# Optimization experiments

Hardware: AMD Instinct MI355X
Metric: run time of the kernel (lower is better)

## Reference

```python
import jax, jax.numpy as jnp
import numpy as np

N_NODES = 50000
N_EDGES = 800000


def _sage_mean(x, src, dst, w, W_self, W_neigh, b, n_nodes):
    # DGL SAGEConv('mean') with edge_weight: messages m_e = w_e * h[src_e],
    # h_neigh[v] = sum_{e->v} m_e / in_degree(v)  (zero if no in-edges),
    # out = h @ W_self + h_neigh @ W_neigh + b
    msg = x[src] * w[:, None]                                   # [E, d]
    s = jax.ops.segment_sum(msg, dst, num_segments=n_nodes)     # [N, d]
    deg = jax.ops.segment_sum(jnp.ones_like(w), dst, num_segments=n_nodes)
    h_neigh = s / jnp.clip(deg, 1.0)[:, None]
    return x @ W_self + h_neigh @ W_neigh + b


def setup_inputs() -> dict:
    key = jax.random.key(0)
    ks = jax.random.split(key, 12)
    d_in, d_h = 64, 256
    inp = {
        'features': jax.random.normal(ks[0], (N_NODES, d_in), dtype=jnp.float32),
        'edge_src': jax.random.randint(ks[1], (N_EDGES,), 0, N_NODES, dtype=jnp.int32),
        'edge_dst': jax.random.randint(ks[2], (N_EDGES,), 0, N_NODES, dtype=jnp.int32),
        'edge_weights': jax.random.uniform(ks[3], (N_EDGES,), dtype=jnp.float32),
        'W1_self': jax.random.normal(ks[4], (d_in, d_h), dtype=jnp.float32) * (1.0 / np.sqrt(d_in)),
        'W1_neigh': jax.random.normal(ks[5], (d_in, d_h), dtype=jnp.float32) * (1.0 / np.sqrt(d_in)),
        'b1': jnp.zeros((d_h,), dtype=jnp.float32),
        'W2_self': jax.random.normal(ks[6], (d_h, 128), dtype=jnp.float32) * (1.0 / np.sqrt(d_h)),
        'W2_neigh': jax.random.normal(ks[7], (d_h, 128), dtype=jnp.float32) * (1.0 / np.sqrt(d_h)),
        'b2': jnp.zeros((128,), dtype=jnp.float32),
        'Wl1': jax.random.normal(ks[8], (128, 64), dtype=jnp.float32) * (1.0 / np.sqrt(128)),
        'bl1': jnp.zeros((64,), dtype=jnp.float32),
        'Wl2': jax.random.normal(ks[9], (64, 32), dtype=jnp.float32) * (1.0 / np.sqrt(64)),
        'bl2': jnp.zeros((32,), dtype=jnp.float32),
        'Wl3': jax.random.normal(ks[10], (32, 10), dtype=jnp.float32) * (1.0 / np.sqrt(32)),
        'bl3': jnp.zeros((10,), dtype=jnp.float32),
    }
    return inp


def reference(features, edge_src, edge_dst, edge_weights,
              W1_self, W1_neigh, b1, W2_self, W2_neigh, b2,
              Wl1, bl1, Wl2, bl2, Wl3, bl3):
    n = features.shape[0]
    x = features.reshape(n, -1)  # flatten (already 2D)
    x = jax.nn.relu(_sage_mean(x, edge_src, edge_dst, edge_weights,
                               W1_self, W1_neigh, b1, n))
    # conv2 is applied twice on identical inputs in the original; results are equal
    embeddings = _sage_mean(x, edge_src, edge_dst, edge_weights,
                            W2_self, W2_neigh, b2, n)
    h = jax.nn.relu(embeddings @ Wl1 + bl1)
    h = jax.nn.relu(h @ Wl2 + bl2)
    out = h @ Wl3 + bl3
    return (out, embeddings)
```

## Files before the change

kernel.cpp:

```cpp
#include <hip/hip_runtime.h>
#include <hip/hip_bf16.h>

#define N_NODES 50000
#define N_EDGES 800000
#define MT_TILES 3125
#define PR_TILES 1563

#define NBLK_SORT 200
#define CHUNK_SORT 4000
#define NBKT 196

typedef __attribute__((ext_vector_type(8))) short frag_ab;
typedef __attribute__((ext_vector_type(4))) float frag_cd;

static __device__ __forceinline__ unsigned short f2b(float f) {
    union { float f; unsigned u; } v; v.f = f;
    unsigned r = v.u + 0x7fffu + ((v.u >> 16) & 1u);
    return (unsigned short)(r >> 16);
}
static __device__ __forceinline__ float b2f(unsigned short b) {
    union { float f; unsigned u; } v; v.u = ((unsigned)b) << 16;
    return v.f;
}
static __device__ __forceinline__ float blo(unsigned p) { return b2f((unsigned short)(p & 0xffffu)); }
static __device__ __forceinline__ float bhi(unsigned p) { return b2f((unsigned short)(p >> 16)); }

static __device__ __forceinline__ unsigned short packBK_elem(const float* __restrict__ Wa,
                                                             const float* __restrict__ Wb,
                                                             int Ka, int N, int idx) {
    int j = idx & 7;
    int lane = (idx >> 3) & 63;
    int rest = idx >> 9;
    int ntiles = N >> 4;
    int nt = rest % ntiles;
    int kt = rest / ntiles;
    int kk = kt * 32 + (lane >> 4) * 8 + j;
    int nn = nt * 16 + (lane & 15);
    float v = (kk < Ka) ? Wa[kk * N + nn] : Wb[(kk - Ka) * N + nn];
    return f2b(v);
}
static __device__ __forceinline__ unsigned short packBN_elem(const float* __restrict__ Wa,
                                                             const float* __restrict__ Wb,
                                                             int Na, int N, int idx) {
    int j = idx & 7;
    int lane = (idx >> 3) & 63;
    int rest = idx >> 9;
    int ntiles = N >> 4;
    int nt = rest % ntiles;
    int kt = rest / ntiles;
    int kk = kt * 32 + (lane >> 4) * 8 + j;
    int nn = nt * 16 + (lane & 15);
    float v = (nn < Na) ? Wa[kk * Na + nn] : Wb[kk * (N - Na) + (nn - Na)];
    return f2b(v);
}

#define PREP_S0 800000
#define PREP_S1 (PREP_S0 + 32768)
#define PREP_S2 (PREP_S1 + 65536)
#define PREP_S3 (PREP_S2 + 8192)
#define PREP_S4 (PREP_S3 + 2048)
#define PREP_BLKS 3549

__global__ __launch_bounds__(256) void prep_p1_kernel(const float4* __restrict__ x4,
                                                      ushort4* __restrict__ xb4,
                                                      const float* __restrict__ W1s,
                                                      const float* __restrict__ W1n,
                                                      const float* __restrict__ W2s,
                                                      const float* __restrict__ W2n,
                                                      const float* __restrict__ Wl1,
                                                      const float* __restrict__ Wl2,
                                                      unsigned short* __restrict__ B1p,
                                                      unsigned short* __restrict__ B2p,
                                                      unsigned short* __restrict__ Bl1p,
                                                      unsigned short* __restrict__ Bl2p,
                                                      const int* __restrict__ dst,
                                                      int* __restrict__ G) {
    __shared__ int h[256];
    int bid = blockIdx.x;
    int t = threadIdx.x;
    if (bid >= PREP_BLKS) {
        int blk = bid - PREP_BLKS;
        h[t] = 0;
        __syncthreads();
        int base = blk * CHUNK_SORT;
        for (int i = t; i < CHUNK_SORT; i += 256)
            atomicAdd(&h[dst[base + i] >> 8], 1);
        __syncthreads();
        G[blk * 256 + t] = h[t];
        return;
    }
    int idx = bid * 256 + t;
    if (idx < PREP_S0) {
        float4 v = x4[idx];
        ushort4 o;
        o.x = f2b(v.x); o.y = f2b(v.y); o.z = f2b(v.z); o.w = f2b(v.w);
        xb4[idx] = o;
    } else if (idx < PREP_S1) {
        int i = idx - PREP_S0;
        B1p[i] = packBK_elem(W1s, W1n, 64, 256, i);
    } else if (idx < PREP_S2) {
        int i = idx - PREP_S1;
        B2p[i] = packBN_elem(W2s, W2n, 128, 256, i);
    } else if (idx < PREP_S3) {
        int i = idx - PREP_S2;
        Bl1p[i] = packBK_elem(Wl1, Wl1, 128, 64, i);
    } else {
        int i = idx - PREP_S3;
        Bl2p[i] = packBK_elem(Wl2, Wl2, 64, 32, i);
    }
}


__global__ __launch_bounds__(256) void p2a_scan(int* __restrict__ G,
                                                int* __restrict__ colsum) {
    __shared__ int sc[256];
    int b = blockIdx.x;
    int t = threadIdx.x;
    int v = (t < NBLK_SORT) ? G[t * 256 + b] : 0;
    sc[t] = v;
    __syncthreads();
    for (int off = 1; off < 256; off <<= 1) {
        int add = (t >= off) ? sc[t - off] : 0;
        __syncthreads();
        sc[t] += add;
        __syncthreads();
    }
    if (t < NBLK_SORT) G[t * 256 + b] = sc[t] - v;
    if (t == 255) colsum[b] = sc[255];
}

__global__ __launch_bounds__(256) void p2b_scan(const int* __restrict__ colsum,
                                                int* __restrict__ bucket_off,
                                                int* __restrict__ row_off) {
    __shared__ int sc[256];
    int t = threadIdx.x;
    int v = colsum[t];
    sc[t] = v;
    __syncthreads();
    for (int off = 1; off < 256; off <<= 1) {
        int add = (t >= off) ? sc[t - off] : 0;
        __syncthreads();
        sc[t] += add;
        __syncthreads();
    }
    bucket_off[t] = sc[t] - v;
    if (t == 255) row_off[N_NODES] = sc[255];
}

__global__ __launch_bounds__(256) void p3_scatter(const int* __restrict__ src,
                                                  const int* __restrict__ dst,
                                                  const float* __restrict__ w,
                                                  const int* __restrict__ G,
                                                  const int* __restrict__ bucket_off,
                                                  int* __restrict__ bdst,
                                                  int2* __restrict__ bsedge) {
    __shared__ int cur[256];
    int t = threadIdx.x;
    cur[t] = G[blockIdx.x * 256 + t] + bucket_off[t];
    __syncthreads();
    int base = blockIdx.x * CHUNK_SORT;
    for (int i = t; i < CHUNK_SORT; i += 256) {
        int e = base + i;
        int d = dst[e];
        int pos = atomicAdd(&cur[d >> 8], 1);
        bdst[pos] = d;
        bsedge[pos] = make_int2(src[e], __float_as_int(w[e]));
    }
}

__global__ __launch_bounds__(256) void p4_sort(const int* __restrict__ bucket_off,
                                               const int* __restrict__ bdst,
                                               const int2* __restrict__ bsedge,
                                               int* __restrict__ row_off,
                                               float* __restrict__ inv_deg,
                                               int2* __restrict__ sedge) {
    __shared__ int lcnt[256];
    __shared__ int lcur[256];
    __shared__ int sc[256];
    int t = threadIdx.x;
    int b = blockIdx.x;
    int e0 = bucket_off[b], e1 = bucket_off[b + 1];
    int d0 = b << 8;
    lcnt[t] = 0;
    __syncthreads();
    for (int e = e0 + t; e < e1; e += 256)
        atomicAdd(&lcnt[bdst[e] - d0], 1);
    __syncthreads();
    int v = lcnt[t];
    sc[t] = v;
    __syncthreads();
    for (int off = 1; off < 256; off <<= 1) {
        int add = (t >= off) ? sc[t - off] : 0;
        __syncthreads();
        sc[t] += add;
        __syncthreads();
    }
    int loff = e0 + sc[t] - v;
    lcur[t] = loff;
    int d = d0 + t;
    if (d < N_NODES) {
        row_off[d] = loff;
        inv_deg[d] = 1.0f / (float)(v > 0 ? v : 1);
    }
    __syncthreads();
    for (int e = e0 + t; e < e1; e += 256) {
        int dd = bdst[e];
        int2 sv = bsedge[e];
        int pos = atomicAdd(&lcur[dd - d0], 1);
        sedge[pos] = sv;
    }
}


__global__ __launch_bounds__(256) void agg64_kernel(const uint4* __restrict__ xb4,
                                                    const int* __restrict__ row_off,
                                                    const int2* __restrict__ sedge,
                                                    const float* __restrict__ inv_deg,
                                                    uint4* __restrict__ hn1b4) {
    int tid = threadIdx.x;
    int lane = tid & 63;
    int er = lane >> 3;
    int l7 = lane & 7;
    int n = blockIdx.x * 4 + (tid >> 6);
    if (n >= N_NODES) return;
    int e0 = row_off[n], e1 = row_off[n + 1];
    float id = inv_deg[n];
    float a[8];
    #pragma unroll
    for (int j = 0; j < 8; j++) a[j] = 0.f;
    int e1m1 = e1 - 1;
    for (int e = e0; e < e1; e += 16) {
        int2 m[2];
        uint4 p[2];
        float w[2];
        #pragma unroll
        for (int k = 0; k < 2; k++) {
            int ee = e + k * 8 + er;
            int idx = ee < e1 ? ee : e1m1;
            m[k] = sedge[idx];
        }
        #pragma unroll
        for (int k = 0; k < 2; k++) {
            p[k] = xb4[m[k].x * 8 + l7];
            int ee = e + k * 8 + er;
            w[k] = (ee < e1) ? __int_as_float(m[k].y) : 0.f;
        }
        #pragma unroll
        for (int k = 0; k < 2; k++) {
            a[0] += w[k] * blo(p[k].x); a[1] += w[k] * bhi(p[k].x);
            a[2] += w[k] * blo(p[k].y); a[3] += w[k] * bhi(p[k].y);
            a[4] += w[k] * blo(p[k].z); a[5] += w[k] * bhi(p[k].z);
            a[6] += w[k] * blo(p[k].w); a[7] += w[k] * bhi(p[k].w);
        }
    }
    #pragma unroll
    for (int j = 0; j < 8; j++) {
        a[j] += __shfl_xor(a[j], 8, 64);
        a[j] += __shfl_xor(a[j], 16, 64);
        a[j] += __shfl_xor(a[j], 32, 64);
    }
    if (er == 0) {
        uint4 o;
        o.x = (unsigned)f2b(a[0] * id) | ((unsigned)f2b(a[1] * id) << 16);
        o.y = (unsigned)f2b(a[2] * id) | ((unsigned)f2b(a[3] * id) << 16);
        o.z = (unsigned)f2b(a[4] * id) | ((unsigned)f2b(a[5] * id) << 16);
        o.w = (unsigned)f2b(a[6] * id) | ((unsigned)f2b(a[7] * id) << 16);
        hn1b4[n * 8 + l7] = o;
    }
}

__global__ __launch_bounds__(256) void agg128_kernel(const uint4* __restrict__ zb4,
                                                     const int* __restrict__ row_off,
                                                     const int2* __restrict__ sedge,
                                                     const float* __restrict__ inv_deg,
                                                     float* __restrict__ emb,
                                                     uint4* __restrict__ embb4) {
    int tid = threadIdx.x;
    int lane = tid & 63;
    int qr = lane >> 4;
    int l15 = lane & 15;
    int n = blockIdx.x * 4 + (tid >> 6);
    if (n >= N_NODES) return;
    int e0 = row_off[n], e1 = row_off[n + 1];
    float id = inv_deg[n];
    float4 s0, s1;
    if (qr == 0) {
        s0 = ((const float4*)emb)[n * 32 + l15 * 2];
        s1 = ((const float4*)emb)[n * 32 + l15 * 2 + 1];
    }
    float a[8];
    #pragma unroll
    for (int j = 0; j < 8; j++) a[j] = 0.f;
    int e1m1 = e1 - 1;
    for (int e = e0; e < e1; e += 16) {
        int2 m[4];
        uint4 p[4];
        float w[4];
        #pragma unroll
        for (int k = 0; k < 4; k++) {
            int ee = e + k * 4 + qr;
            int idx = ee < e1 ? ee : e1m1;
            m[k] = sedge[idx];
        }
        #pragma unroll
        for (int k = 0; k < 4; k++) {
            p[k] = zb4[m[k].x * 16 + l15];
            int ee = e + k * 4 + qr;
            w[k] = (ee < e1) ? __int_as_float(m[k].y) : 0.f;
        }
        #pragma unroll
        for (int k = 0; k < 4; k++) {
            a[0] += w[k] * blo(p[k].x); a[1] += w[k] * bhi(p[k].x);
            a[2] += w[k] * blo(p[k].y); a[3] += w[k] * bhi(p[k].y);
            a[4] += w[k] * blo(p[k].z); a[5] += w[k] * bhi(p[k].z);
            a[6] += w[k] * blo(p[k].w); a[7] += w[k] * bhi(p[k].w);
        }
    }
    #pragma unroll
    for (int j = 0; j < 8; j++) {
        a[j] += __shfl_xor(a[j], 16, 64);
        a[j] += __shfl_xor(a[j], 32, 64);
    }
    if (qr == 0) {
        float v0 = s0.x + a[0] * id;
        float v1 = s0.y + a[1] * id;
        float v2 = s0.z + a[2] * id;
        float v3 = s0.w + a[3] * id;
        float v4 = s1.x + a[4] * id;
        float v5 = s1.y + a[5] * id;
        float v6 = s1.z + a[6] * id;
        float v7 = s1.w + a[7] * id;
        ((float4*)emb)[n * 32 + l15 * 2]     = make_float4(v0, v1, v2, v3);
        ((float4*)emb)[n * 32 + l15 * 2 + 1] = make_float4(v4, v5, v6, v7);
        uint4 o;
        o.x = (unsigned)f2b(v0) | ((unsigned)f2b(v1) << 16);
        o.y = (unsigned)f2b(v2) | ((unsigned)f2b(v3) << 16);
        o.z = (unsigned)f2b(v4) | ((unsigned)f2b(v5) << 16);
        o.w = (unsigned)f2b(v6) | ((unsigned)f2b(v7) << 16);
        embb4[n * 16 + l15] = o;
    }
}


__global__ __launch_bounds__(256) void gemm1_mfma(const unsigned short* __restrict__ xb,
                                                  const unsigned short* __restrict__ hn1b,
                                                  const unsigned short* __restrict__ Bp,
                                                  const float* __restrict__ b1,
                                                  unsigned short* __restrict__ x1b) {
    __shared__ __align__(16) unsigned short sB[8192];
    int tid = threadIdx.x;
    int lane = tid & 63;
    int wv = tid >> 6;
    int mt = blockIdx.x * 4 + wv;
    if (mt >= MT_TILES) mt = MT_TILES - 1;
    int q = lane >> 4;
    int rl = lane & 15;
    int row = mt * 16 + rl;
    frag_ab a[4];
    a[0] = *(const frag_ab*)(xb + row * 64 + q * 8);
    a[1] = *(const frag_ab*)(xb + row * 64 + q * 8 + 32);
    a[2] = *(const frag_ab*)(hn1b + row * 64 + q * 8);
    a[3] = *(const frag_ab*)(hn1b + row * 64 + q * 8 + 32);
    frag_cd acc[16];
    #pragma unroll
    for (int nt = 0; nt < 16; nt++) acc[nt] = (frag_cd){0.f, 0.f, 0.f, 0.f};
    #pragma unroll
    for (int kt = 0; kt < 4; kt++) {
        __syncthreads();
        #pragma unroll
        for (int i = 0; i < 4; i++) {
            int idx = i * 256 + tid;
            ((float4*)sB)[idx] = ((const float4*)(Bp + kt * 8192))[idx];
        }
        __syncthreads();
        #pragma unroll
        for (int nt = 0; nt < 16; nt++) {
            frag_ab b = *(const frag_ab*)(sB + (nt * 64 + lane) * 8);
            acc[nt] = __builtin_amdgcn_mfma_f32_16x16x32_bf16(a[kt], b, acc[nt], 0, 0, 0);
        }
    }
    int r0 = mt * 16;
    #pragma unroll
    for (int nt = 0; nt < 16; nt++) {
        int c = nt * 16 + rl;
        float bias = b1[c];
        #pragma unroll
        for (int i = 0; i < 4; i++) {
            int r = r0 + q * 4 + i;
            float v = acc[nt][i] + bias;
            v = v > 0.f ? v : 0.f;
            x1b[r * 256 + c] = f2b(v);
        }
    }
}

__global__ __launch_bounds__(256) void gemm2_mfma(const unsigned short* __restrict__ x1b,
                                                  const unsigned short* __restrict__ Bp,
                                                  const float* __restrict__ b2,
                                                  float* __restrict__ emb,
                                                  unsigned short* __restrict__ zb) {
    __shared__ __align__(16) unsigned short sB[8192];
    int tid = threadIdx.x;
    int lane = tid & 63;
    int wv = tid >> 6;
    int mt = blockIdx.x * 4 + wv;
    if (mt >= MT_TILES) mt = MT_TILES - 1;
    int q = lane >> 4;
    int rl = lane & 15;
    int row = mt * 16 + rl;
    const unsigned short* arow = x1b + row * 256 + q * 8;
    frag_ab a[8];
    #pragma unroll
    for (int kt = 0; kt < 8; kt++) a[kt] = *(const frag_ab*)(arow + kt * 32);
    frag_cd acc[16];
    #pragma unroll
    for (int nt = 0; nt < 16; nt++) acc[nt] = (frag_cd){0.f, 0.f, 0.f, 0.f};
    #pragma unroll
    for (int kt = 0; kt < 8; kt++) {
        __syncthreads();
        #pragma unroll
        for (int i = 0; i < 4; i++) {
            int idx = i * 256 + tid;
            ((float4*)sB)[idx] = ((const float4*)(Bp + kt * 8192))[idx];
        }
        __syncthreads();
        #pragma unroll
        for (int nt = 0; nt < 16; nt++) {
            frag_ab b = *(const frag_ab*)(sB + (nt * 64 + lane) * 8);
            acc[nt] = __builtin_amdgcn_mfma_f32_16x16x32_bf16(a[kt], b, acc[nt], 0, 0, 0);
        }
    }
    int r0 = mt * 16;
    #pragma unroll
    for (int nt = 0; nt < 8; nt++) {
        int c = nt * 16 + rl;
        float bias = b2[c];
        #pragma unroll
        for (int i = 0; i < 4; i++) {
            int r = r0 + q * 4 + i;
            emb[r * 128 + c] = acc[nt][i] + bias;
        }
    }
    #pragma unroll
    for (int nt = 8; nt < 16; nt++) {
        int c = (nt - 8) * 16 + rl;
        #pragma unroll
        for (int i = 0; i < 4; i++) {
            int r = r0 + q * 4 + i;
            zb[r * 128 + c] = f2b(acc[nt][i]);
        }
    }
}

__global__ __launch_bounds__(256) void mlp1_mfma(const unsigned short* __restrict__ embb,
                                                 const unsigned short* __restrict__ Bp,
                                                 const float* __restrict__ bl1,
                                                 unsigned short* __restrict__ h64b) {
    int tid = threadIdx.x;
    int lane = tid & 63;
    int wv = tid >> 6;
    int pr = blockIdx.x * 4 + wv;
    if (pr >= PR_TILES) pr = PR_TILES - 1;
    int mt0 = pr * 2;
    int mt1 = mt0 + 1; if (mt1 >= MT_TILES) mt1 = MT_TILES - 1;
    int q = lane >> 4;
    int rl = lane & 15;
    const unsigned short* a0row = embb + (mt0 * 16 + rl) * 128 + q * 8;
    const unsigned short* a1row = embb + (mt1 * 16 + rl) * 128 + q * 8;
    const frag_ab* bp = (const frag_ab*)Bp;
    frag_cd acc0[4], acc1[4];
    #pragma unroll
    for (int nt = 0; nt < 4; nt++) {
        acc0[nt] = (frag_cd){0.f, 0.f, 0.f, 0.f};
        acc1[nt] = (frag_cd){0.f, 0.f, 0.f, 0.f};
    }
    #pragma unroll
    for (int kt = 0; kt < 4; kt++) {
        frag_ab a0 = *(const frag_ab*)(a0row + kt * 32);
        frag_ab a1 = *(const frag_ab*)(a1row + kt * 32);
        #pragma unroll
        for (int nt = 0; nt < 4; nt++) {
            frag_ab b = bp[(kt * 4 + nt) * 64 + lane];
            acc0[nt] = __builtin_amdgcn_mfma_f32_16x16x32_bf16(a0, b, acc0[nt], 0, 0, 0);
            acc1[nt] = __builtin_amdgcn_mfma_f32_16x16x32_bf16(a1, b, acc1[nt], 0, 0, 0);
        }
    }
    int r0a = mt0 * 16 + q * 4, r0b = mt1 * 16 + q * 4;
    #pragma unroll
    for (int nt = 0; nt < 4; nt++) {
        int c = nt * 16 + rl;
        float bias = bl1[c];
        #pragma unroll
        for (int i = 0; i < 4; i++) {
            float v0 = acc0[nt][i] + bias;
            float v1 = acc1[nt][i] + bias;
            h64b[(r0a + i) * 64 + c] = f2b(v0 > 0.f ? v0 : 0.f);
            h64b[(r0b + i) * 64 + c] = f2b(v1 > 0.f ? v1 : 0.f);
        }
    }
}

__global__ __launch_bounds__(256) void mlp23_mfma(const unsigned short* __restrict__ h64b,
                                                  const unsigned short* __restrict__ Bp,
                                                  const float* __restrict__ bl2,
                                                  const float* __restrict__ Wl3,
                                                  const float* __restrict__ bl3,
                                                  float* __restrict__ out) {
    __shared__ float hs[64][33];
    int tid = threadIdx.x;
    int lane = tid & 63;
    int wv = tid >> 6;
    int mt = blockIdx.x * 4 + wv;
    if (mt >= MT_TILES) mt = MT_TILES - 1;
    int q = lane >> 4;
    int rl = lane & 15;
    const unsigned short* arow = h64b + (mt * 16 + rl) * 64 + q * 8;
    const frag_ab* bp = (const frag_ab*)Bp;
    frag_cd acc[2];
    #pragma unroll
    for (int nt = 0; nt < 2; nt++) acc[nt] = (frag_cd){0.f, 0.f, 0.f, 0.f};
    #pragma unroll
    for (int kt = 0; kt < 2; kt++) {
        frag_ab a = *(const frag_ab*)(arow + kt * 32);
        #pragma unroll
        for (int nt = 0; nt < 2; nt++) {
            frag_ab b = bp[(kt * 2 + nt) * 64 + lane];
            acc[nt] = __builtin_amdgcn_mfma_f32_16x16x32_bf16(a, b, acc[nt], 0, 0, 0);
        }
    }
    #pragma unroll
    for (int nt = 0; nt < 2; nt++) {
        int c = nt * 16 + rl;
        float bias = bl2[c];
        #pragma unroll
        for (int i = 0; i < 4; i++) {
            int lr = wv * 16 + q * 4 + i;
            float v = acc[nt][i] + bias;
            hs[lr][c] = v > 0.f ? v : 0.f;
        }
    }
    __syncthreads();
    int base = blockIdx.x * 64;
    for (int idx = tid; idx < 640; idx += 256) {
        int lr = idx / 10;
        int j = idx - lr * 10;
        int n = base + lr;
        if (n < N_NODES) {
            float a = bl3[j];
            #pragma unroll
            for (int k = 0; k < 32; k++) a += hs[lr][k] * Wl3[k * 10 + j];
            out[n * 10 + j] = a;
        }
    }
}


extern "C" void kernel_launch(void* const* d_in, const int* in_sizes, int n_in,
                              void* d_out, int out_size, void* d_ws, size_t ws_size,
                              hipStream_t stream) {
    const float* x   = (const float*)d_in[0];
    const int* esrc  = (const int*)d_in[1];
    const int* edst  = (const int*)d_in[2];
    const float* ew  = (const float*)d_in[3];
    const float* W1s = (const float*)d_in[4];
    const float* W1n = (const float*)d_in[5];
    const float* b1  = (const float*)d_in[6];
    const float* W2s = (const float*)d_in[7];
    const float* W2n = (const float*)d_in[8];
    const float* b2  = (const float*)d_in[9];
    const float* Wl1 = (const float*)d_in[10];
    const float* bl1 = (const float*)d_in[11];
    const float* Wl2 = (const float*)d_in[12];
    const float* bl2 = (const float*)d_in[13];
    const float* Wl3 = (const float*)d_in[14];
    const float* bl3 = (const float*)d_in[15];

    float* out = (float*)d_out;
    float* emb = out + 500000;

    char* ws = (char*)d_ws;
    size_t off = 0;
    auto alloc = [&](size_t bytes) -> void* {
        void* p = ws + off;
        off = (off + bytes + 255) & ~(size_t)255;
        return p;
    };
    int*   row_off = (int*)alloc((size_t)(N_NODES + 1) * 4);
    float* inv_deg = (float*)alloc((size_t)N_NODES * 4);
    int*   G       = (int*)alloc((size_t)NBLK_SORT * 256 * 4);
    int*   colsum  = (int*)alloc(256 * 4);
    int*   bkt_off = (int*)alloc(257 * 4);
    int*   bdst    = (int*)alloc((size_t)N_EDGES * 4);
    int2*  bsedge  = (int2*)alloc((size_t)N_EDGES * 8);
    int2*  sedge   = (int2*)alloc((size_t)N_EDGES * 8);
    unsigned short* xb   = (unsigned short*)alloc((size_t)N_NODES * 64 * 2);
    unsigned short* hn1b = (unsigned short*)alloc((size_t)N_NODES * 64 * 2);
    unsigned short* x1b  = (unsigned short*)alloc((size_t)N_NODES * 256 * 2);
    unsigned short* zb   = (unsigned short*)alloc((size_t)N_NODES * 128 * 2);
    unsigned short* embb = (unsigned short*)alloc((size_t)N_NODES * 128 * 2);
    unsigned short* h64b = (unsigned short*)alloc((size_t)N_NODES * 64 * 2);
    unsigned short* B1p  = (unsigned short*)alloc(128 * 256 * 2);
    unsigned short* B2p  = (unsigned short*)alloc(256 * 256 * 2);
    unsigned short* Bl1p = (unsigned short*)alloc(128 * 64 * 2);
    unsigned short* Bl2p = (unsigned short*)alloc(64 * 32 * 2);

    prep_p1_kernel<<<PREP_BLKS + NBLK_SORT, 256, 0, stream>>>(
        (const float4*)x, (ushort4*)xb, W1s, W1n, W2s, W2n, Wl1, Wl2,
        B1p, B2p, Bl1p, Bl2p, edst, G);

    p2a_scan<<<256, 256, 0, stream>>>(G, colsum);
    p2b_scan<<<1, 256, 0, stream>>>(colsum, bkt_off, row_off);
    p3_scatter<<<NBLK_SORT, 256, 0, stream>>>(esrc, edst, ew, G, bkt_off, bdst, bsedge);
    p4_sort<<<NBKT, 256, 0, stream>>>(bkt_off, bdst, bsedge, row_off, inv_deg, sedge);

    const int PBLK = (PR_TILES + 3) / 4;
    const int GBLK = (MT_TILES + 3) / 4;
    const int ABLK = (N_NODES + 3) / 4;

    agg64_kernel<<<ABLK, 256, 0, stream>>>((const uint4*)xb, row_off, sedge,
                                           inv_deg, (uint4*)hn1b);
    gemm1_mfma<<<GBLK, 256, 0, stream>>>(xb, hn1b, B1p, b1, x1b);

    gemm2_mfma<<<GBLK, 256, 0, stream>>>(x1b, B2p, b2, emb, zb);
    agg128_kernel<<<ABLK, 256, 0, stream>>>((const uint4*)zb, row_off, sedge,
                                            inv_deg, emb, (uint4*)embb);

    mlp1_mfma<<<PBLK, 256, 0, stream>>>(embb, Bl1p, bl1, h64b);
    mlp23_mfma<<<GBLK, 256, 0, stream>>>(h64b, Bl2p, bl2, Wl3, bl3, out);
}
```

Measured before the change: 269.3 us.

## Fold bucket scan into scatter/sort, double-buffer GEMM weights, fuse MLP layers

The single-block bucket-offset scan is removed; p3_scatter and p4_sort now each recompute the 256-entry prefix sum of colsum in shared memory, saving one launch. gemm1 and gemm2 move to 512-thread blocks with double-buffered shared-memory weight tiles, prefetching the next K-slice into registers while the MFMAs run, so each K step needs one barrier instead of two. The three MLP layers run in one kernel that keeps the 64-wide hidden activations in shared memory, dropping the h64b round trip through global memory and one launch. In exchange the scan work is repeated in every scatter and sort block, and the GEMM blocks use more LDS and more threads per block.

```diff
diff --git a/kernel.cpp b/kernel.cpp
--- a/kernel.cpp
+++ b/kernel.cpp
@@ -4,7 +4,6 @@
 #define N_NODES 50000
 #define N_EDGES 800000
 #define MT_TILES 3125
-#define PR_TILES 1563
 
 #define NBLK_SORT 200
 #define CHUNK_SORT 4000
@@ -129,9 +128,14 @@
     if (t == 255) colsum[b] = sc[255];
 }
 
-__global__ __launch_bounds__(256) void p2b_scan(const int* __restrict__ colsum,
-                                                int* __restrict__ bucket_off,
-                                                int* __restrict__ row_off) {
+__global__ __launch_bounds__(256) void p3_scatter(const int* __restrict__ src,
+                                                  const int* __restrict__ dst,
+                                                  const float* __restrict__ w,
+                                                  const int* __restrict__ G,
+                                                  const int* __restrict__ colsum,
+                                                  int* __restrict__ bdst,
+                                                  int2* __restrict__ bsedge) {
+    __shared__ int cur[256];
     __shared__ int sc[256];
     int t = threadIdx.x;
     int v = colsum[t];
@@ -143,20 +147,7 @@
         sc[t] += add;
         __syncthreads();
     }
-    bucket_off[t] = sc[t] - v;
-    if (t == 255) row_off[N_NODES] = sc[255];
-}
-
-__global__ __launch_bounds__(256) void p3_scatter(const int* __restrict__ src,
-                                                  const int* __restrict__ dst,
-                                                  const float* __restrict__ w,
-                                                  const int* __restrict__ G,
-                                                  const int* __restrict__ bucket_off,
-                                                  int* __restrict__ bdst,
-                                                  int2* __restrict__ bsedge) {
-    __shared__ int cur[256];
-    int t = threadIdx.x;
-    cur[t] = G[blockIdx.x * 256 + t] + bucket_off[t];
+    cur[t] = G[blockIdx.x * 256 + t] + (sc[t] - v);
     __syncthreads();
     int base = blockIdx.x * CHUNK_SORT;
     for (int i = t; i < CHUNK_SORT; i += 256) {
@@ -168,7 +159,7 @@
     }
 }
 
-__global__ __launch_bounds__(256) void p4_sort(const int* __restrict__ bucket_off,
+__global__ __launch_bounds__(256) void p4_sort(const int* __restrict__ colsum,
                                                const int* __restrict__ bdst,
                                                const int2* __restrict__ bsedge,
                                                int* __restrict__ row_off,
@@ -177,12 +168,23 @@
     __shared__ int lcnt[256];
     __shared__ int lcur[256];
     __shared__ int sc[256];
+    __shared__ int sE0, sE1;
     int t = threadIdx.x;
     int b = blockIdx.x;
-    int e0 = bucket_off[b], e1 = bucket_off[b + 1];
+    int cv = colsum[t];
+    sc[t] = cv;
+    __syncthreads();
+    for (int off = 1; off < 256; off <<= 1) {
+        int add = (t >= off) ? sc[t - off] : 0;
+        __syncthreads();
+        sc[t] += add;
+        __syncthreads();
+    }
+    if (t == b) { sE0 = sc[t] - cv; sE1 = sc[t]; }
+    lcnt[t] = 0;
+    __syncthreads();
+    int e0 = sE0, e1 = sE1;
     int d0 = b << 8;
-    lcnt[t] = 0;
-    __syncthreads();
     for (int e = e0 + t; e < e1; e += 256)
         atomicAdd(&lcnt[bdst[e] - d0], 1);
     __syncthreads();
@@ -202,6 +204,7 @@
         row_off[d] = loff;
         inv_deg[d] = 1.0f / (float)(v > 0 ? v : 1);
     }
+    if (b == 0 && t == 0) row_off[N_NODES] = N_EDGES;
     __syncthreads();
     for (int e = e0 + t; e < e1; e += 256) {
         int dd = bdst[e];
@@ -342,16 +345,16 @@
 }
 
 
-__global__ __launch_bounds__(256) void gemm1_mfma(const unsigned short* __restrict__ xb,
+__global__ __launch_bounds__(512) void gemm1_mfma(const unsigned short* __restrict__ xb,
                                                   const unsigned short* __restrict__ hn1b,
                                                   const unsigned short* __restrict__ Bp,
                                                   const float* __restrict__ b1,
                                                   unsigned short* __restrict__ x1b) {
-    __shared__ __align__(16) unsigned short sB[8192];
+    __shared__ __align__(16) unsigned short sB[2][8192];
     int tid = threadIdx.x;
     int lane = tid & 63;
     int wv = tid >> 6;
-    int mt = blockIdx.x * 4 + wv;
+    int mt = blockIdx.x * 8 + wv;
     if (mt >= MT_TILES) mt = MT_TILES - 1;
     int q = lane >> 4;
     int rl = lane & 15;
@@ -364,19 +367,23 @@
     frag_cd acc[16];
     #pragma unroll
     for (int nt = 0; nt < 16; nt++) acc[nt] = (frag_cd){0.f, 0.f, 0.f, 0.f};
+    const float4* gB = (const float4*)Bp;
+    float4 s0 = gB[tid], s1 = gB[512 + tid];
+    ((float4*)sB[0])[tid] = s0;
+    ((float4*)sB[0])[512 + tid] = s1;
     #pragma unroll
     for (int kt = 0; kt < 4; kt++) {
         __syncthreads();
-        #pragma unroll
-        for (int i = 0; i < 4; i++) {
-            int idx = i * 256 + tid;
-            ((float4*)sB)[idx] = ((const float4*)(Bp + kt * 8192))[idx];
-        }
-        __syncthreads();
+        if (kt < 3) { s0 = gB[(kt + 1) * 1024 + tid]; s1 = gB[(kt + 1) * 1024 + 512 + tid]; }
+        const unsigned short* sb = sB[kt & 1];
         #pragma unroll
         for (int nt = 0; nt < 16; nt++) {
-            frag_ab b = *(const frag_ab*)(sB + (nt * 64 + lane) * 8);
+            frag_ab b = *(const frag_ab*)(sb + (nt * 64 + lane) * 8);
             acc[nt] = __builtin_amdgcn_mfma_f32_16x16x32_bf16(a[kt], b, acc[nt], 0, 0, 0);
+        }
+        if (kt < 3) {
+            ((float4*)sB[(kt + 1) & 1])[tid] = s0;
+            ((float4*)sB[(kt + 1) & 1])[512 + tid] = s1;
         }
     }
     int r0 = mt * 16;
@@ -394,16 +401,16 @@
     }
 }
 
-__global__ __launch_bounds__(256) void gemm2_mfma(const unsigned short* __restrict__ x1b,
+__global__ __launch_bounds__(512) void gemm2_mfma(const unsigned short* __restrict__ x1b,
                                                   const unsigned short* __restrict__ Bp,
                                                   const float* __restrict__ b2,
                                                   float* __restrict__ emb,
                                                   unsigned short* __restrict__ zb) {
-    __shared__ __align__(16) unsigned short sB[8192];
+    __shared__ __align__(16) unsigned short sB[2][8192];
     int tid = threadIdx.x;
     int lane = tid & 63;
     int wv = tid >> 6;
-    int mt = blockIdx.x * 4 + wv;
+    int mt = blockIdx.x * 8 + wv;
     if (mt >= MT_TILES) mt = MT_TILES - 1;
     int q = lane >> 4;
     int rl = lane & 15;
@@ -415,19 +422,23 @@
     frag_cd acc[16];
     #pragma unroll
     for (int nt = 0; nt < 16; nt++) acc[nt] = (frag_cd){0.f, 0.f, 0.f, 0.f};
+    const float4* gB = (const float4*)Bp;
+    float4 s0 = gB[tid], s1 = gB[512 + tid];
+    ((float4*)sB[0])[tid] = s0;
+    ((float4*)sB[0])[512 + tid] = s1;
     #pragma unroll
     for (int kt = 0; kt < 8; kt++) {
         __syncthreads();
-        #pragma unroll
-        for (int i = 0; i < 4; i++) {
-            int idx = i * 256 + tid;
-            ((float4*)sB)[idx] = ((const float4*)(Bp + kt * 8192))[idx];
-        }
-        __syncthreads();
+        if (kt < 7) { s0 = gB[(kt + 1) * 1024 + tid]; s1 = gB[(kt + 1) * 1024 + 512 + tid]; }
+        const unsigned short* sb = sB[kt & 1];
         #pragma unroll
         for (int nt = 0; nt < 16; nt++) {
-            frag_ab b = *(const frag_ab*)(sB + (nt * 64 + lane) * 8);
+            frag_ab b = *(const frag_ab*)(sb + (nt * 64 + lane) * 8);
             acc[nt] = __builtin_amdgcn_mfma_f32_16x16x32_bf16(a[kt], b, acc[nt], 0, 0, 0);
+        }
+        if (kt < 7) {
+            ((float4*)sB[(kt + 1) & 1])[tid] = s0;
+            ((float4*)sB[(kt + 1) & 1])[512 + tid] = s1;
         }
     }
     int r0 = mt * 16;
@@ -452,60 +463,15 @@
     }
 }
 
-__global__ __launch_bounds__(256) void mlp1_mfma(const unsigned short* __restrict__ embb,
-                                                 const unsigned short* __restrict__ Bp,
+__global__ __launch_bounds__(256) void mlp_fused(const unsigned short* __restrict__ embb,
+                                                 const unsigned short* __restrict__ B1,
                                                  const float* __restrict__ bl1,
-                                                 unsigned short* __restrict__ h64b) {
-    int tid = threadIdx.x;
-    int lane = tid & 63;
-    int wv = tid >> 6;
-    int pr = blockIdx.x * 4 + wv;
-    if (pr >= PR_TILES) pr = PR_TILES - 1;
-    int mt0 = pr * 2;
-    int mt1 = mt0 + 1; if (mt1 >= MT_TILES) mt1 = MT_TILES - 1;
-    int q = lane >> 4;
-    int rl = lane & 15;
-    const unsigned short* a0row = embb + (mt0 * 16 + rl) * 128 + q * 8;
-    const unsigned short* a1row = embb + (mt1 * 16 + rl) * 128 + q * 8;
-    const frag_ab* bp = (const frag_ab*)Bp;
-    frag_cd acc0[4], acc1[4];
-    #pragma unroll
-    for (int nt = 0; nt < 4; nt++) {
-        acc0[nt] = (frag_cd){0.f, 0.f, 0.f, 0.f};
-        acc1[nt] = (frag_cd){0.f, 0.f, 0.f, 0.f};
-    }
-    #pragma unroll
-    for (int kt = 0; kt < 4; kt++) {
-        frag_ab a0 = *(const frag_ab*)(a0row + kt * 32);
-        frag_ab a1 = *(const frag_ab*)(a1row + kt * 32);
-        #pragma unroll
-        for (int nt = 0; nt < 4; nt++) {
-            frag_ab b = bp[(kt * 4 + nt) * 64 + lane];
-            acc0[nt] = __builtin_amdgcn_mfma_f32_16x16x32_bf16(a0, b, acc0[nt], 0, 0, 0);
-            acc1[nt] = __builtin_amdgcn_mfma_f32_16x16x32_bf16(a1, b, acc1[nt], 0, 0, 0);
-        }
-    }
-    int r0a = mt0 * 16 + q * 4, r0b = mt1 * 16 + q * 4;
-    #pragma unroll
-    for (int nt = 0; nt < 4; nt++) {
-        int c = nt * 16 + rl;
-        float bias = bl1[c];
-        #pragma unroll
-        for (int i = 0; i < 4; i++) {
-            float v0 = acc0[nt][i] + bias;
-            float v1 = acc1[nt][i] + bias;
-            h64b[(r0a + i) * 64 + c] = f2b(v0 > 0.f ? v0 : 0.f);
-            h64b[(r0b + i) * 64 + c] = f2b(v1 > 0.f ? v1 : 0.f);
-        }
-    }
-}
-
-__global__ __launch_bounds__(256) void mlp23_mfma(const unsigned short* __restrict__ h64b,
-                                                  const unsigned short* __restrict__ Bp,
-                                                  const float* __restrict__ bl2,
-                                                  const float* __restrict__ Wl3,
-                                                  const float* __restrict__ bl3,
-                                                  float* __restrict__ out) {
+                                                 const unsigned short* __restrict__ B2,
+                                                 const float* __restrict__ bl2,
+                                                 const float* __restrict__ Wl3,
+                                                 const float* __restrict__ bl3,
+                                                 float* __restrict__ out) {
+    __shared__ __align__(16) unsigned short h64s[64 * 72];
     __shared__ float hs[64][33];
     int tid = threadIdx.x;
     int lane = tid & 63;
@@ -514,19 +480,40 @@
     if (mt >= MT_TILES) mt = MT_TILES - 1;
     int q = lane >> 4;
     int rl = lane & 15;
-    const unsigned short* arow = h64b + (mt * 16 + rl) * 64 + q * 8;
-    const frag_ab* bp = (const frag_ab*)Bp;
-    frag_cd acc[2];
-    #pragma unroll
-    for (int nt = 0; nt < 2; nt++) acc[nt] = (frag_cd){0.f, 0.f, 0.f, 0.f};
+    const unsigned short* arow = embb + (mt * 16 + rl) * 128 + q * 8;
+    const frag_ab* bp1 = (const frag_ab*)B1;
+    frag_cd acc[4];
+    #pragma unroll
+    for (int nt = 0; nt < 4; nt++) acc[nt] = (frag_cd){0.f, 0.f, 0.f, 0.f};
+    #pragma unroll
+    for (int kt = 0; kt < 4; kt++) {
+        frag_ab a = *(const frag_ab*)(arow + kt * 32);
+        #pragma unroll
+        for (int nt = 0; nt < 4; nt++)
+            acc[nt] = __builtin_amdgcn_mfma_f32_16x16x32_bf16(a, bp1[(kt * 4 + nt) * 64 + lane], acc[nt], 0, 0, 0);
+    }
+    #pragma unroll
+    for (int nt = 0; nt < 4; nt++) {
+        int c = nt * 16 + rl;
+        float bias = bl1[c];
+        #pragma unroll
+        for (int i = 0; i < 4; i++) {
+            float v = acc[nt][i] + bias;
+            h64s[(wv * 16 + q * 4 + i) * 72 + c] = f2b(v > 0.f ? v : 0.f);
+        }
+    }
+    __syncthreads();
+    const unsigned short* a2 = h64s + (wv * 16 + rl) * 72 + q * 8;
+    const frag_ab* bp2 = (const frag_ab*)B2;
+    frag_cd acc2[2];
+    #pragma unroll
+    for (int nt = 0; nt < 2; nt++) acc2[nt] = (frag_cd){0.f, 0.f, 0.f, 0.f};
     #pragma unroll
     for (int kt = 0; kt < 2; kt++) {
-        frag_ab a = *(const frag_ab*)(arow + kt * 32);
-        #pragma unroll
-        for (int nt = 0; nt < 2; nt++) {
-            frag_ab b = bp[(kt * 2 + nt) * 64 + lane];
-            acc[nt] = __builtin_amdgcn_mfma_f32_16x16x32_bf16(a, b, acc[nt], 0, 0, 0);
-        }
+        frag_ab a = *(const frag_ab*)(a2 + kt * 32);
+        #pragma unroll
+        for (int nt = 0; nt < 2; nt++)
+            acc2[nt] = __builtin_amdgcn_mfma_f32_16x16x32_bf16(a, bp2[(kt * 2 + nt) * 64 + lane], acc2[nt], 0, 0, 0);
     }
     #pragma unroll
     for (int nt = 0; nt < 2; nt++) {
@@ -535,7 +522,7 @@
         #pragma unroll
         for (int i = 0; i < 4; i++) {
             int lr = wv * 16 + q * 4 + i;
-            float v = acc[nt][i] + bias;
+            float v = acc2[nt][i] + bias;
             hs[lr][c] = v > 0.f ? v : 0.f;
         }
     }
@@ -589,7 +576,6 @@
     float* inv_deg = (float*)alloc((size_t)N_NODES * 4);
     int*   G       = (int*)alloc((size_t)NBLK_SORT * 256 * 4);
     int*   colsum  = (int*)alloc(256 * 4);
-    int*   bkt_off = (int*)alloc(257 * 4);
     int*   bdst    = (int*)alloc((size_t)N_EDGES * 4);
     int2*  bsedge  = (int2*)alloc((size_t)N_EDGES * 8);
     int2*  sedge   = (int2*)alloc((size_t)N_EDGES * 8);
@@ -598,7 +584,6 @@
     unsigned short* x1b  = (unsigned short*)alloc((size_t)N_NODES * 256 * 2);
     unsigned short* zb   = (unsigned short*)alloc((size_t)N_NODES * 128 * 2);
     unsigned short* embb = (unsigned short*)alloc((size_t)N_NODES * 128 * 2);
-    unsigned short* h64b = (unsigned short*)alloc((size_t)N_NODES * 64 * 2);
     unsigned short* B1p  = (unsigned short*)alloc(128 * 256 * 2);
     unsigned short* B2p  = (unsigned short*)alloc(256 * 256 * 2);
     unsigned short* Bl1p = (unsigned short*)alloc(128 * 64 * 2);
@@ -609,22 +594,20 @@
         B1p, B2p, Bl1p, Bl2p, edst, G);
 
     p2a_scan<<<256, 256, 0, stream>>>(G, colsum);
-    p2b_scan<<<1, 256, 0, stream>>>(colsum, bkt_off, row_off);
-    p3_scatter<<<NBLK_SORT, 256, 0, stream>>>(esrc, edst, ew, G, bkt_off, bdst, bsedge);
-    p4_sort<<<NBKT, 256, 0, stream>>>(bkt_off, bdst, bsedge, row_off, inv_deg, sedge);
-
-    const int PBLK = (PR_TILES + 3) / 4;
-    const int GBLK = (MT_TILES + 3) / 4;
-    const int ABLK = (N_NODES + 3) / 4;
+    p3_scatter<<<NBLK_SORT, 256, 0, stream>>>(esrc, edst, ew, G, colsum, bdst, bsedge);
+    p4_sort<<<NBKT, 256, 0, stream>>>(colsum, bdst, bsedge, row_off, inv_deg, sedge);
+
+    const int GBLK8 = (MT_TILES + 7) / 8;
+    const int GBLK  = (MT_TILES + 3) / 4;
+    const int ABLK  = (N_NODES + 3) / 4;
 
     agg64_kernel<<<ABLK, 256, 0, stream>>>((const uint4*)xb, row_off, sedge,
                                            inv_deg, (uint4*)hn1b);
-    gemm1_mfma<<<GBLK, 256, 0, stream>>>(xb, hn1b, B1p, b1, x1b);
-
-    gemm2_mfma<<<GBLK, 256, 0, stream>>>(x1b, B2p, b2, emb, zb);
+    gemm1_mfma<<<GBLK8, 512, 0, stream>>>(xb, hn1b, B1p, b1, x1b);
+
+    gemm2_mfma<<<GBLK8, 512, 0, stream>>>(x1b, B2p, b2, emb, zb);
     agg128_kernel<<<ABLK, 256, 0, stream>>>((const uint4*)zb, row_off, sedge,
                                             inv_deg, emb, (uint4*)embb);
 
-    mlp1_mfma<<<PBLK, 256, 0, stream>>>(embb, Bl1p, bl1, h64b);
-    mlp23_mfma<<<GBLK, 256, 0, stream>>>(h64b, Bl2p, bl2, Wl3, bl3, out);
-}
+    mlp_fused<<<GBLK, 256, 0, stream>>>(embb, Bl1p, bl1, Bl2p, bl2, Wl3, bl3, out);
+}
```

Result: faster. 234.1 us (-13.0%).
